# Kernel optimization log

Measured on AMD Instinct MI355X. Metric: run time of the kernel, lower is better.

## Reference

```python
import jax, jax.numpy as jnp
import numpy as np

N = 50000      # num_nodes
SEQ = 52       # seq_len (weeks)
FIN = 16       # in_channels
H = 128        # hidden_dim
E = 800000     # num edges (before self-loops)
NEG_SLOPE = 0.2


def setup_inputs() -> dict:
    key = jax.random.key(0)
    ks = jax.random.split(key, 10)
    return {
        "x_seq": jax.random.normal(ks[0], (SEQ, N, FIN), jnp.float32),
        "edge_index": jax.random.randint(ks[1], (2, E), 0, N),
        "Wg": jax.random.normal(ks[2], (FIN, H), jnp.float32) * 0.1,       # GAT linear (no bias on lin in PyG default path; bias added at end)
        "att_src": jax.random.normal(ks[3], (H,), jnp.float32) * 0.1,
        "att_dst": jax.random.normal(ks[4], (H,), jnp.float32) * 0.1,
        "bias_g": jnp.zeros((H,), jnp.float32),
        "W_ih": jax.random.normal(ks[5], (3 * H, H), jnp.float32) * 0.05,  # GRUCell input weights (r,z,n order)
        "W_hh": jax.random.normal(ks[6], (3 * H, H), jnp.float32) * 0.05,
        "b_ih": jnp.zeros((3 * H,), jnp.float32),
        "b_hh": jnp.zeros((3 * H,), jnp.float32),
        "W_fc": jax.random.normal(ks[7], (1, H), jnp.float32) * 0.1,
        "b_fc": jnp.zeros((1,), jnp.float32),
    }


def _gat(x, src, dst, Wg, att_src, att_dst, bias_g):
    # x: [N, FIN] -> xp: [N, H]
    xp = x @ Wg
    a_s = xp @ att_src  # [N]
    a_d = xp @ att_dst  # [N]
    e = jax.nn.leaky_relu(a_s[src] + a_d[dst], NEG_SLOPE)          # [E+N] edge scores
    m = jax.ops.segment_max(e, dst, num_segments=N)                # softmax over incoming edges per dst
    w = jnp.exp(e - m[dst])
    denom = jax.ops.segment_sum(w, dst, num_segments=N)
    alpha = w / denom[dst]
    out = jax.ops.segment_sum(alpha[:, None] * xp[src], dst, num_segments=N)  # [N, H]
    return out + bias_g


def _gru_cell(x, h, W_ih, W_hh, b_ih, b_hh):
    gi = x @ W_ih.T + b_ih  # [N, 3H]
    gh = h @ W_hh.T + b_hh
    i_r, i_z, i_n = jnp.split(gi, 3, axis=1)
    h_r, h_z, h_n = jnp.split(gh, 3, axis=1)
    r = jax.nn.sigmoid(i_r + h_r)
    z = jax.nn.sigmoid(i_z + h_z)
    n = jnp.tanh(i_n + r * h_n)
    return (1.0 - z) * n + z * h


def reference(x_seq, edge_index, Wg, att_src, att_dst, bias_g, W_ih, W_hh, b_ih, b_hh, W_fc, b_fc):
    # PyG GATConv add_self_loops=True
    loop = jnp.arange(N)
    src = jnp.concatenate([edge_index[0], loop])
    dst = jnp.concatenate([edge_index[1], loop])

    def step(h, xt):
        spatial = jax.nn.relu(_gat(xt, src, dst, Wg, att_src, att_dst, bias_g))
        h_new = _gru_cell(spatial, h, W_ih, W_hh, b_ih, b_hh)
        return h_new, None

    h0 = jnp.zeros((N, H), jnp.float32)
    hT, _ = jax.lax.scan(step, h0, x_seq)
    return hT @ W_fc.T + b_fc  # [N, 1]
```

## Files before the change

kernel.cpp:

```cpp
#include <hip/hip_runtime.h>
#include <math.h>

#define NN 50000
#define SEQ 52
#define FIN 16
#define HD 128
#define NEG_SLOPE 0.2f

typedef short bf16x8 __attribute__((ext_vector_type(8)));
typedef float f32x16 __attribute__((ext_vector_type(16)));

__device__ __forceinline__ short f2bf(float x) {
    unsigned u = __float_as_uint(x);
    u += 0x7fffu + ((u >> 16) & 1u);
    return (short)(u >> 16);
}
__device__ __forceinline__ float b2f(short s) {
    return __uint_as_float(((unsigned)(unsigned short)s) << 16);
}

__global__ void deg_init_kernel(int* deg, int n) {
    int i = blockIdx.x * blockDim.x + threadIdx.x;
    if (i < n) deg[i] = 1;
}

__global__ void deg_count_kernel(const int* __restrict__ dst, int* deg, int e) {
    int i = blockIdx.x * blockDim.x + threadIdx.x;
    if (i < e) atomicAdd(&deg[dst[i]], 1);
}

__global__ __launch_bounds__(1024) void scan_kernel(const int* __restrict__ deg,
                                                    int* row_ptr, int n) {
    __shared__ int buf[1024];
    __shared__ int carry;
    int tid = threadIdx.x;
    if (tid == 0) carry = 0;
    __syncthreads();
    for (int base = 0; base < n; base += 1024) {
        int i = base + tid;
        int v = (i < n) ? deg[i] : 0;
        buf[tid] = v;
        __syncthreads();
        for (int off = 1; off < 1024; off <<= 1) {
            int t = (tid >= off) ? buf[tid - off] : 0;
            __syncthreads();
            buf[tid] += t;
            __syncthreads();
        }
        if (i < n) row_ptr[i] = carry + buf[tid] - v;
        __syncthreads();
        if (tid == 1023) carry += buf[1023];
        __syncthreads();
    }
    if (tid == 0) row_ptr[n] = carry;
}

__global__ void selfloop_kernel(const int* __restrict__ row_ptr, int* cursor,
                                int* col, int n) {
    int i = blockIdx.x * blockDim.x + threadIdx.x;
    if (i < n) {
        int p = row_ptr[i];
        col[p] = i;
        cursor[i] = p + 1;
    }
}

__global__ void scatter_kernel(const int* __restrict__ src, const int* __restrict__ dst,
                               int* cursor, int* col, int e) {
    int i = blockIdx.x * blockDim.x + threadIdx.x;
    if (i < e) {
        int p = atomicAdd(&cursor[dst[i]], 1);
        col[p] = src[i];
    }
}

__global__ void wpack_kernel(const float* __restrict__ Wi, const float* __restrict__ Wh,
                             short* __restrict__ wfrag) {
    int idx = blockIdx.x * blockDim.x + threadIdx.x;
    if (idx >= 3 * 4 * 8 * 4 * 64) return;
    int lane = idx & 63;
    int which = (idx >> 6) & 3;
    int ks = (idx >> 8) & 7;
    int slab = (idx >> 11) & 3;
    int g = idx >> 13;
    int col = slab * 32 + (lane & 31);
    int kcol = ks * 16 + (lane >> 5) * 8;
    const float* Wsrc = (which < 2) ? Wi : Wh;
    const float* row = Wsrc + (size_t)(g * HD + col) * HD + kcol;
    short* dstp = wfrag + (size_t)idx * 8;
    bool lo = (which & 1);
#pragma unroll
    for (int e = 0; e < 8; ++e) {
        float v = row[e];
        short hi = f2bf(v);
        dstp[e] = lo ? f2bf(v - b2f(hi)) : hi;
    }
}


__global__ __launch_bounds__(256) void xp_kernel(
    const float* __restrict__ x, const float* __restrict__ Wg,
    const float* __restrict__ att_src, const float* __restrict__ att_dst,
    unsigned* __restrict__ xpb, float* __restrict__ a_s, float* __restrict__ a_d, int n) {
    int wave = (blockIdx.x * blockDim.x + threadIdx.x) >> 6;
    int lane = threadIdx.x & 63;
    if (wave >= n) return;
    const float* xr = x + (size_t)wave * FIN;
    float xv[FIN];
#pragma unroll
    for (int k = 0; k < FIN; ++k) xv[k] = xr[k];
    int c0 = 2 * lane, c1 = 2 * lane + 1;
    float v0 = 0.f, v1 = 0.f;
#pragma unroll
    for (int k = 0; k < FIN; ++k) {
        v0 += xv[k] * Wg[k * HD + c0];
        v1 += xv[k] * Wg[k * HD + c1];
    }
    unsigned p = (unsigned)(unsigned short)f2bf(v0) |
                 ((unsigned)(unsigned short)f2bf(v1) << 16);
    xpb[(size_t)wave * 64 + lane] = p;
    float s = v0 * att_src[c0] + v1 * att_src[c1];
    float d = v0 * att_dst[c0] + v1 * att_dst[c1];
#pragma unroll
    for (int off = 32; off; off >>= 1) {
        s += __shfl_xor(s, off);
        d += __shfl_xor(d, off);
    }
    if (lane == 0) { a_s[wave] = s; a_d[wave] = d; }
}

__global__ __launch_bounds__(256, 4) void gatgru_kernel(
    const int* __restrict__ row_ptr, const int* __restrict__ col,
    const float* __restrict__ a_s, const float* __restrict__ a_d,
    const short* __restrict__ xpb, const float* __restrict__ bias_g,
    float* __restrict__ h, const short* __restrict__ wfrag,
    const float* __restrict__ b_ih, const float* __restrict__ b_hh, int n,
    const float* __restrict__ x_next, const float* __restrict__ Wg,
    const float* __restrict__ att_src, const float* __restrict__ att_dst,
    unsigned* __restrict__ xpb_next, float* __restrict__ a_s_next,
    float* __restrict__ a_d_next) {
    __shared__ bf16x8 sSH[512];
    __shared__ bf16x8 sSL[512];
    __shared__ bf16x8 sHH[512];
    __shared__ bf16x8 sHL[512];

    int t = threadIdx.x;
    int lane = t & 63;
    int w = t >> 6;
    int n0 = blockIdx.x * 32;

    float h8[2][8];
#pragma unroll
    for (int q = 0; q < 2; ++q) {
        int ks = w * 2 + q;
        int row = n0 + (lane & 31);
        if (row >= n) row = n - 1;
        int kcol = ks * 16 + (lane >> 5) * 8;
        const float* hp = h + (size_t)row * HD + kcol;
        *(float4*)(h8[q]) = *(const float4*)(hp);
        *(float4*)(h8[q] + 4) = *(const float4*)(hp + 4);
    }

    int g = t >> 4;
    int fg = t & 15;
    int glane = lane & 0x30;

#pragma unroll
    for (int nn = 0; nn < 2; ++nn) {
        int nl = g + nn * 16;
        int nd = n0 + nl;
        int sidx = (fg >> 1) * 64 + (fg & 1) * 32 + nl;
        if (nd < n) {
            int start = row_ptr[nd], end = row_ptr[nd + 1];
            float ad = a_d[nd];
            float acc[8] = {0.f, 0.f, 0.f, 0.f, 0.f, 0.f, 0.f, 0.f};
            float dpart = 0.f;
            for (int base = start; base < end; base += 16) {
                int cnt = end - base;
                if (cnt > 16) cnt = 16;
                int s = 0;
                float wgt = 0.f;
                if (fg < cnt) {
                    s = col[base + fg];
                    float e = a_s[s] + ad;
                    e = (e > 0.f) ? e : NEG_SLOPE * e;
                    wgt = __expf(e);
                }
                dpart += wgt;
                for (int k = 0; k < cnt; k += 4) {
                    int si[4];
                    float wt[4];
#pragma unroll
                    for (int u = 0; u < 4; ++u) {
                        int c = k + u;
                        int cc = (c < cnt) ? c : 0;
                        si[u] = __shfl(s, glane | cc);
                        wt[u] = __shfl(wgt, glane | cc);
                        if (c >= cnt) wt[u] = 0.f;
                    }
                    bf16x8 r[4];
#pragma unroll
                    for (int u = 0; u < 4; ++u)
                        r[u] = *(const bf16x8*)(xpb + (size_t)si[u] * HD + fg * 8);
#pragma unroll
                    for (int u = 0; u < 4; ++u)
#pragma unroll
                        for (int j = 0; j < 8; ++j) acc[j] += wt[u] * b2f(r[u][j]);
                }
            }
            dpart += __shfl_xor(dpart, 8);
            dpart += __shfl_xor(dpart, 4);
            dpart += __shfl_xor(dpart, 2);
            dpart += __shfl_xor(dpart, 1);
            float inv = __fdividef(1.f, dpart);
            bf16x8 sh, sl;
#pragma unroll
            for (int j = 0; j < 8; ++j) {
                float o = acc[j] * inv + bias_g[fg * 8 + j];
                o = fmaxf(o, 0.f);
                short hi = f2bf(o);
                sh[j] = hi;
                sl[j] = f2bf(o - b2f(hi));
            }
            sSH[sidx] = sh;
            sSL[sidx] = sl;
        } else {
            bf16x8 z;
#pragma unroll
            for (int j = 0; j < 8; ++j) z[j] = 0;
            sSH[sidx] = z;
            sSL[sidx] = z;
        }
    }

#pragma unroll
    for (int q = 0; q < 2; ++q) {
        int ks = w * 2 + q;
        bf16x8 hh, hl;
#pragma unroll
        for (int j = 0; j < 8; ++j) {
            short b = f2bf(h8[q][j]);
            hh[j] = b;
            hl[j] = f2bf(h8[q][j] - b2f(b));
        }
        int li = ks * 64 + lane;
        sHH[li] = hh;
        sHL[li] = hl;
    }
    __syncthreads();

    int j0 = w * 32;
    int cj = lane & 31;
    int kh = lane >> 5;

    const short* wb = wfrag + (size_t)w * 16384 + (size_t)lane * 8;

    f32x16 arz0, arz1;
#pragma unroll
    for (int r = 0; r < 16; ++r) { arz0[r] = 0.f; arz1[r] = 0.f; }

#pragma unroll
    for (int ks = 0; ks < 8; ++ks) {
        int li = ks * 64 + lane;
        bf16x8 aSH = sSH[li];
        bf16x8 aSL = sSL[li];
        bf16x8 aHH = sHH[li];
        bf16x8 aHL = sHL[li];
        {
            const short* p = wb + 0 * 65536 + ks * 2048;
            bf16x8 wih = *(const bf16x8*)(p);
            bf16x8 wil = *(const bf16x8*)(p + 512);
            bf16x8 whh = *(const bf16x8*)(p + 1024);
            bf16x8 whl = *(const bf16x8*)(p + 1536);
            arz0 = __builtin_amdgcn_mfma_f32_32x32x16_bf16(aSH, wih, arz0, 0, 0, 0);
            arz0 = __builtin_amdgcn_mfma_f32_32x32x16_bf16(aHH, whh, arz0, 0, 0, 0);
            arz0 = __builtin_amdgcn_mfma_f32_32x32x16_bf16(aSL, wih, arz0, 0, 0, 0);
            arz0 = __builtin_amdgcn_mfma_f32_32x32x16_bf16(aHL, whh, arz0, 0, 0, 0);
            arz0 = __builtin_amdgcn_mfma_f32_32x32x16_bf16(aSH, wil, arz0, 0, 0, 0);
            arz0 = __builtin_amdgcn_mfma_f32_32x32x16_bf16(aHH, whl, arz0, 0, 0, 0);
        }
        {
            const short* p = wb + 1 * 65536 + ks * 2048;
            bf16x8 wih = *(const bf16x8*)(p);
            bf16x8 wil = *(const bf16x8*)(p + 512);
            bf16x8 whh = *(const bf16x8*)(p + 1024);
            bf16x8 whl = *(const bf16x8*)(p + 1536);
            arz1 = __builtin_amdgcn_mfma_f32_32x32x16_bf16(aSH, wih, arz1, 0, 0, 0);
            arz1 = __builtin_amdgcn_mfma_f32_32x32x16_bf16(aHH, whh, arz1, 0, 0, 0);
            arz1 = __builtin_amdgcn_mfma_f32_32x32x16_bf16(aSL, wih, arz1, 0, 0, 0);
            arz1 = __builtin_amdgcn_mfma_f32_32x32x16_bf16(aHL, whh, arz1, 0, 0, 0);
            arz1 = __builtin_amdgcn_mfma_f32_32x32x16_bf16(aSH, wil, arz1, 0, 0, 0);
            arz1 = __builtin_amdgcn_mfma_f32_32x32x16_bf16(aHH, whl, arz1, 0, 0, 0);
        }
    }

    f32x16 ain, ahn;
#pragma unroll
    for (int r = 0; r < 16; ++r) { ain[r] = 0.f; ahn[r] = 0.f; }

#pragma unroll
    for (int ks = 0; ks < 8; ++ks) {
        int li = ks * 64 + lane;
        bf16x8 aSH = sSH[li];
        bf16x8 aSL = sSL[li];
        bf16x8 aHH = sHH[li];
        bf16x8 aHL = sHL[li];
        const short* p = wb + 2 * 65536 + ks * 2048;
        bf16x8 wih = *(const bf16x8*)(p);
        bf16x8 wil = *(const bf16x8*)(p + 512);
        bf16x8 whh = *(const bf16x8*)(p + 1024);
        bf16x8 whl = *(const bf16x8*)(p + 1536);
        ain = __builtin_amdgcn_mfma_f32_32x32x16_bf16(aSH, wih, ain, 0, 0, 0);
        ahn = __builtin_amdgcn_mfma_f32_32x32x16_bf16(aHH, whh, ahn, 0, 0, 0);
        ain = __builtin_amdgcn_mfma_f32_32x32x16_bf16(aSL, wih, ain, 0, 0, 0);
        ahn = __builtin_amdgcn_mfma_f32_32x32x16_bf16(aHL, whh, ahn, 0, 0, 0);
        ain = __builtin_amdgcn_mfma_f32_32x32x16_bf16(aSH, wil, ain, 0, 0, 0);
        ahn = __builtin_amdgcn_mfma_f32_32x32x16_bf16(aHH, whl, ahn, 0, 0, 0);
    }

    int j = j0 + cj;
    float brz0 = b_ih[j] + b_hh[j];
    float brz1 = b_ih[HD + j] + b_hh[HD + j];
    float bin_ = b_ih[2 * HD + j];
    float bhn = b_hh[2 * HD + j];
    const short* hhs = (const short*)sHH;
    const short* hls = (const short*)sHL;
    int ksj = j >> 4, halfj = (j >> 3) & 1, ej = j & 7;

#pragma unroll
    for (int r = 0; r < 16; ++r) {
        int nl = (r & 3) + 8 * (r >> 2) + 4 * kh;
        int node = n0 + nl;
        if (node < n) {
            float rr = __fdividef(1.f, 1.f + __expf(-(arz0[r] + brz0)));
            float zz = __fdividef(1.f, 1.f + __expf(-(arz1[r] + brz1)));
            float u = ain[r] + bin_ + rr * (ahn[r] + bhn);
            float ex = __expf(2.f * u);
            float nn2 = 1.f - __fdividef(2.f, ex + 1.f);
            int li = (ksj * 64 + nl + 32 * halfj) * 8 + ej;
            float hold = b2f(hhs[li]) + b2f(hls[li]);
            h[(size_t)node * HD + j] = (1.f - zz) * nn2 + zz * hold;
        }
    }

    if (x_next != nullptr) {
        int node = n0 + (t >> 3);
        int sub = t & 7;
        if (node < n) {
            const float* xr = x_next + (size_t)node * FIN;
            float xv[FIN];
#pragma unroll
            for (int k = 0; k < FIN; ++k) xv[k] = xr[k];
            float s = 0.f, d = 0.f;
            unsigned pk[8];
#pragma unroll
            for (int c = 0; c < 16; c += 2) {
                int c0 = sub * 16 + c, c1 = c0 + 1;
                float v0 = 0.f, v1 = 0.f;
#pragma unroll
                for (int k = 0; k < FIN; ++k) {
                    v0 += xv[k] * Wg[k * HD + c0];
                    v1 += xv[k] * Wg[k * HD + c1];
                }
                s += v0 * att_src[c0] + v1 * att_src[c1];
                d += v0 * att_dst[c0] + v1 * att_dst[c1];
                pk[c >> 1] = (unsigned)(unsigned short)f2bf(v0) |
                             ((unsigned)(unsigned short)f2bf(v1) << 16);
            }
            unsigned* dstw = xpb_next + (size_t)node * 64 + sub * 8;
            *(uint4*)(dstw) = make_uint4(pk[0], pk[1], pk[2], pk[3]);
            *(uint4*)(dstw + 4) = make_uint4(pk[4], pk[5], pk[6], pk[7]);
            s += __shfl_xor(s, 1); s += __shfl_xor(s, 2); s += __shfl_xor(s, 4);
            d += __shfl_xor(d, 1); d += __shfl_xor(d, 2); d += __shfl_xor(d, 4);
            if (sub == 0) { a_s_next[node] = s; a_d_next[node] = d; }
        }
    }
}

__global__ __launch_bounds__(256) void fc_kernel(
    const float* __restrict__ h, const float* __restrict__ W_fc,
    const float* __restrict__ b_fc, float* __restrict__ out, int n) {
    int wave = (blockIdx.x * blockDim.x + threadIdx.x) >> 6;
    int lane = threadIdx.x & 63;
    if (wave >= n) return;
    float v = h[(size_t)wave * HD + lane] * W_fc[lane] +
              h[(size_t)wave * HD + lane + 64] * W_fc[lane + 64];
#pragma unroll
    for (int off = 32; off; off >>= 1) v += __shfl_xor(v, off);
    if (lane == 0) out[wave] = v + b_fc[0];
}

extern "C" void kernel_launch(void* const* d_in, const int* in_sizes, int n_in,
                              void* d_out, int out_size, void* d_ws, size_t ws_size,
                              hipStream_t stream) {
    const float* x_seq   = (const float*)d_in[0];
    const int*   ei      = (const int*)d_in[1];
    const float* Wg      = (const float*)d_in[2];
    const float* att_src = (const float*)d_in[3];
    const float* att_dst = (const float*)d_in[4];
    const float* bias_g  = (const float*)d_in[5];
    const float* W_ih    = (const float*)d_in[6];
    const float* W_hh    = (const float*)d_in[7];
    const float* b_ih    = (const float*)d_in[8];
    const float* b_hh    = (const float*)d_in[9];
    const float* W_fc    = (const float*)d_in[10];
    const float* b_fc    = (const float*)d_in[11];
    float* out = (float*)d_out;

    const int N = NN;
    const int E = in_sizes[1] / 2;
    const int* src = ei;
    const int* dst = ei + E;

    char* w = (char*)d_ws;
    size_t off = 0;
    auto alloc = [&](size_t bytes) {
        char* p = w + off;
        off = (off + bytes + 255) & ~(size_t)255;
        return p;
    };
    int*   deg     = (int*)alloc((size_t)N * 4);
    int*   row_ptr = (int*)alloc((size_t)(N + 1) * 4);
    int*   cursor  = (int*)alloc((size_t)N * 4);
    int*   col     = (int*)alloc((size_t)(E + N) * 4);
    float* a_s0    = (float*)alloc((size_t)N * 4);
    float* a_d0    = (float*)alloc((size_t)N * 4);
    float* a_s1    = (float*)alloc((size_t)N * 4);
    float* a_d1    = (float*)alloc((size_t)N * 4);
    unsigned* xpb0 = (unsigned*)alloc((size_t)N * 64 * 4);
    unsigned* xpb1 = (unsigned*)alloc((size_t)N * 64 * 4);
    float* hbuf    = (float*)alloc((size_t)N * HD * 4);
    short* wfrag   = (short*)alloc((size_t)3 * 4 * 8 * 4 * 64 * 8 * 2);

    unsigned* xpbs[2] = {xpb0, xpb1};
    float* a_ss[2] = {a_s0, a_s1};
    float* a_ds[2] = {a_d0, a_d1};

    hipMemsetAsync(hbuf, 0, (size_t)N * HD * 4, stream);

    deg_init_kernel<<<(N + 255) / 256, 256, 0, stream>>>(deg, N);
    deg_count_kernel<<<(E + 255) / 256, 256, 0, stream>>>(dst, deg, E);
    scan_kernel<<<1, 1024, 0, stream>>>(deg, row_ptr, N);
    selfloop_kernel<<<(N + 255) / 256, 256, 0, stream>>>(row_ptr, cursor, col, N);
    scatter_kernel<<<(E + 255) / 256, 256, 0, stream>>>(src, dst, cursor, col, E);
    wpack_kernel<<<(24576 + 255) / 256, 256, 0, stream>>>(W_ih, W_hh, wfrag);

    int node_wave_blocks = (N * 64 + 255) / 256;
    int fused_blocks = (N + 31) / 32;

    xp_kernel<<<node_wave_blocks, 256, 0, stream>>>(x_seq, Wg, att_src, att_dst,
                                                    xpb0, a_s0, a_d0, N);

    for (int t = 0; t < SEQ; ++t) {
        int cur = t & 1, nxt = cur ^ 1;
        const float* xnext = (t + 1 < SEQ) ? (x_seq + (size_t)(t + 1) * N * FIN)
                                           : nullptr;
        gatgru_kernel<<<fused_blocks, 256, 0, stream>>>(
            row_ptr, col, a_ss[cur], a_ds[cur], (const short*)xpbs[cur], bias_g,
            hbuf, wfrag, b_ih, b_hh, N,
            xnext, Wg, att_src, att_dst, xpbs[nxt], a_ss[nxt], a_ds[nxt]);
    }
    fc_kernel<<<node_wave_blocks, 256, 0, stream>>>(hbuf, W_fc, b_fc, out, N);
}
```

Before: 5.701 ms.

## Stage per-block edge weights in LDS once instead of per 16-lane group

At the start of each fused GAT+GRU block, all edges of the block's 32 destination nodes are loaded cooperatively into shared memory as (src, exp score) pairs, using a new dst_slot array built during CSR construction. The aggregation loop then reads indices and weights from LDS instead of recomputing them with per-lane gathers and shuffles, and computes the denominator in-thread. A fallback keeps the old path when a block has more than ECAP edges. The GRU epilogue also reloads the old h from global memory instead of reconstructing it from the bf16 hi/lo LDS copies. This costs extra LDS (6 KB), a block barrier, and an extra global read of dst_slot.

```diff
diff --git a/kernel.cpp b/kernel.cpp
--- a/kernel.cpp
+++ b/kernel.cpp
@@ -6,6 +6,7 @@
 #define FIN 16
 #define HD 128
 #define NEG_SLOPE 0.2f
+#define ECAP 768
 
 typedef short bf16x8 __attribute__((ext_vector_type(8)));
 typedef float f32x16 __attribute__((ext_vector_type(16)));
@@ -56,21 +57,24 @@
 }
 
 __global__ void selfloop_kernel(const int* __restrict__ row_ptr, int* cursor,
-                                int* col, int n) {
+                                int* col, int* dst_slot, int n) {
     int i = blockIdx.x * blockDim.x + threadIdx.x;
     if (i < n) {
         int p = row_ptr[i];
         col[p] = i;
+        dst_slot[p] = i;
         cursor[i] = p + 1;
     }
 }
 
 __global__ void scatter_kernel(const int* __restrict__ src, const int* __restrict__ dst,
-                               int* cursor, int* col, int e) {
+                               int* cursor, int* col, int* dst_slot, int e) {
     int i = blockIdx.x * blockDim.x + threadIdx.x;
     if (i < e) {
-        int p = atomicAdd(&cursor[dst[i]], 1);
+        int d = dst[i];
+        int p = atomicAdd(&cursor[d], 1);
         col[p] = src[i];
+        dst_slot[p] = d;
     }
 }
 
@@ -131,6 +135,7 @@
 
 __global__ __launch_bounds__(256, 4) void gatgru_kernel(
     const int* __restrict__ row_ptr, const int* __restrict__ col,
+    const int* __restrict__ dst_slot,
     const float* __restrict__ a_s, const float* __restrict__ a_d,
     const short* __restrict__ xpb, const float* __restrict__ bias_g,
     float* __restrict__ h, const short* __restrict__ wfrag,
@@ -143,6 +148,7 @@
     __shared__ bf16x8 sSL[512];
     __shared__ bf16x8 sHH[512];
     __shared__ bf16x8 sHL[512];
+    __shared__ uint2  sE[ECAP];
 
     int t = threadIdx.x;
     int lane = t & 63;
@@ -161,6 +167,21 @@
         *(float4*)(h8[q] + 4) = *(const float4*)(hp + 4);
     }
 
+    int nend = (n0 + 32 < n) ? (n0 + 32) : n;
+    int rp0 = row_ptr[n0];
+    int ecnt = row_ptr[nend] - rp0;
+    bool staged = (ecnt <= ECAP);
+    if (staged) {
+        for (int p = t; p < ecnt; p += 256) {
+            int gp = rp0 + p;
+            int s = col[gp];
+            float e = a_s[s] + a_d[dst_slot[gp]];
+            e = (e > 0.f) ? e : NEG_SLOPE * e;
+            sE[p] = make_uint2((unsigned)s, __float_as_uint(__expf(e)));
+        }
+    }
+    __syncthreads();
+
     int g = t >> 4;
     int fg = t & 15;
     int glane = lane & 0x30;
@@ -172,47 +193,75 @@
         int sidx = (fg >> 1) * 64 + (fg & 1) * 32 + nl;
         if (nd < n) {
             int start = row_ptr[nd], end = row_ptr[nd + 1];
-            float ad = a_d[nd];
             float acc[8] = {0.f, 0.f, 0.f, 0.f, 0.f, 0.f, 0.f, 0.f};
-            float dpart = 0.f;
-            for (int base = start; base < end; base += 16) {
-                int cnt = end - base;
-                if (cnt > 16) cnt = 16;
-                int s = 0;
-                float wgt = 0.f;
-                if (fg < cnt) {
-                    s = col[base + fg];
-                    float e = a_s[s] + ad;
-                    e = (e > 0.f) ? e : NEG_SLOPE * e;
-                    wgt = __expf(e);
-                }
-                dpart += wgt;
+            float denom = 0.f;
+            if (staged) {
+                int s0 = start - rp0;
+                int cnt = end - start;
                 for (int k = 0; k < cnt; k += 4) {
                     int si[4];
                     float wt[4];
 #pragma unroll
                     for (int u = 0; u < 4; ++u) {
                         int c = k + u;
-                        int cc = (c < cnt) ? c : 0;
-                        si[u] = __shfl(s, glane | cc);
-                        wt[u] = __shfl(wgt, glane | cc);
-                        if (c >= cnt) wt[u] = 0.f;
+                        uint2 ew = sE[s0 + ((c < cnt) ? c : 0)];
+                        si[u] = (int)ew.x;
+                        wt[u] = (c < cnt) ? __uint_as_float(ew.y) : 0.f;
                     }
                     bf16x8 r[4];
 #pragma unroll
                     for (int u = 0; u < 4; ++u)
                         r[u] = *(const bf16x8*)(xpb + (size_t)si[u] * HD + fg * 8);
 #pragma unroll
-                    for (int u = 0; u < 4; ++u)
+                    for (int u = 0; u < 4; ++u) {
+                        denom += wt[u];
 #pragma unroll
                         for (int j = 0; j < 8; ++j) acc[j] += wt[u] * b2f(r[u][j]);
+                    }
                 }
+            } else {
+                float ad = a_d[nd];
+                float dpart = 0.f;
+                for (int base = start; base < end; base += 16) {
+                    int cnt = end - base;
+                    if (cnt > 16) cnt = 16;
+                    int s = 0;
+                    float wgt = 0.f;
+                    if (fg < cnt) {
+                        s = col[base + fg];
+                        float e = a_s[s] + ad;
+                        e = (e > 0.f) ? e : NEG_SLOPE * e;
+                        wgt = __expf(e);
+                    }
+                    dpart += wgt;
+                    for (int k = 0; k < cnt; k += 4) {
+                        int si[4];
+                        float wt[4];
+#pragma unroll
+                        for (int u = 0; u < 4; ++u) {
+                            int c = k + u;
+                            int cc = (c < cnt) ? c : 0;
+                            si[u] = __shfl(s, glane | cc);
+                            wt[u] = __shfl(wgt, glane | cc);
+                            if (c >= cnt) wt[u] = 0.f;
+                        }
+                        bf16x8 r[4];
+#pragma unroll
+                        for (int u = 0; u < 4; ++u)
+                            r[u] = *(const bf16x8*)(xpb + (size_t)si[u] * HD + fg * 8);
+#pragma unroll
+                        for (int u = 0; u < 4; ++u)
+#pragma unroll
+                            for (int j = 0; j < 8; ++j) acc[j] += wt[u] * b2f(r[u][j]);
+                    }
+                }
+                dpart += __shfl_xor(dpart, 8);
+                dpart += __shfl_xor(dpart, 4);
+                dpart += __shfl_xor(dpart, 2);
+                dpart += __shfl_xor(dpart, 1);
+                denom = dpart;
             }
-            dpart += __shfl_xor(dpart, 8);
-            dpart += __shfl_xor(dpart, 4);
-            dpart += __shfl_xor(dpart, 2);
-            dpart += __shfl_xor(dpart, 1);
-            float inv = __fdividef(1.f, dpart);
+            float inv = __fdividef(1.f, denom);
             bf16x8 sh, sl;
 #pragma unroll
             for (int j = 0; j < 8; ++j) {
@@ -323,22 +372,18 @@
     float brz1 = b_ih[HD + j] + b_hh[HD + j];
     float bin_ = b_ih[2 * HD + j];
     float bhn = b_hh[2 * HD + j];
-    const short* hhs = (const short*)sHH;
-    const short* hls = (const short*)sHL;
-    int ksj = j >> 4, halfj = (j >> 3) & 1, ej = j & 7;
 
 #pragma unroll
     for (int r = 0; r < 16; ++r) {
         int nl = (r & 3) + 8 * (r >> 2) + 4 * kh;
         int node = n0 + nl;
         if (node < n) {
+            float hold = h[(size_t)node * HD + j];
             float rr = __fdividef(1.f, 1.f + __expf(-(arz0[r] + brz0)));
             float zz = __fdividef(1.f, 1.f + __expf(-(arz1[r] + brz1)));
             float u = ain[r] + bin_ + rr * (ahn[r] + bhn);
             float ex = __expf(2.f * u);
             float nn2 = 1.f - __fdividef(2.f, ex + 1.f);
-            int li = (ksj * 64 + nl + 32 * halfj) * 8 + ej;
-            float hold = b2f(hhs[li]) + b2f(hls[li]);
             h[(size_t)node * HD + j] = (1.f - zz) * nn2 + zz * hold;
         }
     }
@@ -419,18 +464,19 @@
         off = (off + bytes + 255) & ~(size_t)255;
         return p;
     };
-    int*   deg     = (int*)alloc((size_t)N * 4);
-    int*   row_ptr = (int*)alloc((size_t)(N + 1) * 4);
-    int*   cursor  = (int*)alloc((size_t)N * 4);
-    int*   col     = (int*)alloc((size_t)(E + N) * 4);
-    float* a_s0    = (float*)alloc((size_t)N * 4);
-    float* a_d0    = (float*)alloc((size_t)N * 4);
-    float* a_s1    = (float*)alloc((size_t)N * 4);
-    float* a_d1    = (float*)alloc((size_t)N * 4);
-    unsigned* xpb0 = (unsigned*)alloc((size_t)N * 64 * 4);
-    unsigned* xpb1 = (unsigned*)alloc((size_t)N * 64 * 4);
-    float* hbuf    = (float*)alloc((size_t)N * HD * 4);
-    short* wfrag   = (short*)alloc((size_t)3 * 4 * 8 * 4 * 64 * 8 * 2);
+    int*   deg      = (int*)alloc((size_t)N * 4);
+    int*   row_ptr  = (int*)alloc((size_t)(N + 1) * 4);
+    int*   cursor   = (int*)alloc((size_t)N * 4);
+    int*   col      = (int*)alloc((size_t)(E + N) * 4);
+    int*   dst_slot = (int*)alloc((size_t)(E + N) * 4);
+    float* a_s0     = (float*)alloc((size_t)N * 4);
+    float* a_d0     = (float*)alloc((size_t)N * 4);
+    float* a_s1     = (float*)alloc((size_t)N * 4);
+    float* a_d1     = (float*)alloc((size_t)N * 4);
+    unsigned* xpb0  = (unsigned*)alloc((size_t)N * 64 * 4);
+    unsigned* xpb1  = (unsigned*)alloc((size_t)N * 64 * 4);
+    float* hbuf     = (float*)alloc((size_t)N * HD * 4);
+    short* wfrag    = (short*)alloc((size_t)3 * 4 * 8 * 4 * 64 * 8 * 2);
 
     unsigned* xpbs[2] = {xpb0, xpb1};
     float* a_ss[2] = {a_s0, a_s1};
@@ -441,8 +487,10 @@
     deg_init_kernel<<<(N + 255) / 256, 256, 0, stream>>>(deg, N);
     deg_count_kernel<<<(E + 255) / 256, 256, 0, stream>>>(dst, deg, E);
     scan_kernel<<<1, 1024, 0, stream>>>(deg, row_ptr, N);
-    selfloop_kernel<<<(N + 255) / 256, 256, 0, stream>>>(row_ptr, cursor, col, N);
-    scatter_kernel<<<(E + 255) / 256, 256, 0, stream>>>(src, dst, cursor, col, E);
+    selfloop_kernel<<<(N + 255) / 256, 256, 0, stream>>>(row_ptr, cursor, col,
+                                                         dst_slot, N);
+    scatter_kernel<<<(E + 255) / 256, 256, 0, stream>>>(src, dst, cursor, col,
+                                                        dst_slot, E);
     wpack_kernel<<<(24576 + 255) / 256, 256, 0, stream>>>(W_ih, W_hh, wfrag);
 
     int node_wave_blocks = (N * 64 + 255) / 256;
@@ -456,8 +504,8 @@
         const float* xnext = (t + 1 < SEQ) ? (x_seq + (size_t)(t + 1) * N * FIN)
                                            : nullptr;
         gatgru_kernel<<<fused_blocks, 256, 0, stream>>>(
-            row_ptr, col, a_ss[cur], a_ds[cur], (const short*)xpbs[cur], bias_g,
-            hbuf, wfrag, b_ih, b_hh, N,
+            row_ptr, col, dst_slot, a_ss[cur], a_ds[cur], (const short*)xpbs[cur],
+            bias_g, hbuf, wfrag, b_ih, b_hh, N,
             xnext, Wg, att_src, att_dst, xpbs[nxt], a_ss[nxt], a_ds[nxt]);
     }
     fc_kernel<<<node_wave_blocks, 256, 0, stream>>>(hbuf, W_fc, b_fc, out, N);
```

After: 6.154 ms. 7.9% more time.

## Bucket each node's incoming edges by source range to improve gather locality

Applied to the files above, without the earlier changes.

Builds the CSR with four sub-rows per destination node, grouped by which quarter of the node ID space the source falls in. The fused GAT/GRU kernel then walks all nodes' edges for source range 0 before moving to range 1, and so on. The aim is to keep the working set of gathered bf16 feature rows within a cache-sized slice at any moment. In exchange, each destination's edges are split into smaller chunks, so the 16-lane groups run less full, there are more loop iterations, and the preprocessing arrays and scan are four times larger.

```diff
diff --git a/kernel.cpp b/kernel.cpp
--- a/kernel.cpp
+++ b/kernel.cpp
@@ -6,6 +6,8 @@
 #define FIN 16
 #define HD 128
 #define NEG_SLOPE 0.2f
+#define NRANGE 4
+#define RDIV 12500
 
 typedef short bf16x8 __attribute__((ext_vector_type(8)));
 typedef float f32x16 __attribute__((ext_vector_type(16)));
@@ -19,14 +21,18 @@
     return __uint_as_float(((unsigned)(unsigned short)s) << 16);
 }
 
-__global__ void deg_init_kernel(int* deg, int n) {
+__global__ void deg_init_kernel(int* deg4, int n4) {
     int i = blockIdx.x * blockDim.x + threadIdx.x;
-    if (i < n) deg[i] = 1;
-}
-
-__global__ void deg_count_kernel(const int* __restrict__ dst, int* deg, int e) {
+    if (i < n4) {
+        int node = i >> 2, r = i & 3;
+        deg4[i] = (r == node / RDIV) ? 1 : 0;
+    }
+}
+
+__global__ void deg_count_kernel(const int* __restrict__ src,
+                                 const int* __restrict__ dst, int* deg4, int e) {
     int i = blockIdx.x * blockDim.x + threadIdx.x;
-    if (i < e) atomicAdd(&deg[dst[i]], 1);
+    if (i < e) atomicAdd(&deg4[dst[i] * 4 + src[i] / RDIV], 1);
 }
 
 __global__ __launch_bounds__(1024) void scan_kernel(const int* __restrict__ deg,
@@ -55,22 +61,28 @@
     if (tid == 0) row_ptr[n] = carry;
 }
 
-__global__ void selfloop_kernel(const int* __restrict__ row_ptr, int* cursor,
-                                int* col, int n) {
+__global__ void selfloop_kernel(const int* __restrict__ row_ptr4, int* cursor4,
+                                int* col, int n4) {
     int i = blockIdx.x * blockDim.x + threadIdx.x;
-    if (i < n) {
-        int p = row_ptr[i];
-        col[p] = i;
-        cursor[i] = p + 1;
+    if (i < n4) {
+        int node = i >> 2, r = i & 3;
+        int base = row_ptr4[i];
+        if (r == node / RDIV) {
+            col[base] = node;
+            cursor4[i] = base + 1;
+        } else {
+            cursor4[i] = base;
+        }
     }
 }
 
 __global__ void scatter_kernel(const int* __restrict__ src, const int* __restrict__ dst,
-                               int* cursor, int* col, int e) {
+                               int* cursor4, int* col, int e) {
     int i = blockIdx.x * blockDim.x + threadIdx.x;
     if (i < e) {
-        int p = atomicAdd(&cursor[dst[i]], 1);
-        col[p] = src[i];
+        int s = src[i];
+        int p = atomicAdd(&cursor4[dst[i] * 4 + s / RDIV], 1);
+        col[p] = s;
     }
 }
 
@@ -130,7 +142,7 @@
 }
 
 __global__ __launch_bounds__(256, 4) void gatgru_kernel(
-    const int* __restrict__ row_ptr, const int* __restrict__ col,
+    const int* __restrict__ rp4, const int* __restrict__ col,
     const float* __restrict__ a_s, const float* __restrict__ a_d,
     const short* __restrict__ xpb, const float* __restrict__ bias_g,
     float* __restrict__ h, const short* __restrict__ wfrag,
@@ -165,58 +177,78 @@
     int fg = t & 15;
     int glane = lane & 0x30;
 
+    float acc[2][8];
+    float dpart[2] = {0.f, 0.f};
+    float adv[2];
+#pragma unroll
+    for (int nn = 0; nn < 2; ++nn) {
+#pragma unroll
+        for (int j = 0; j < 8; ++j) acc[nn][j] = 0.f;
+        int nd = n0 + g + nn * 16;
+        adv[nn] = (nd < n) ? a_d[nd] : 0.f;
+    }
+
+#pragma unroll
+    for (int p = 0; p < NRANGE; ++p) {
+#pragma unroll
+        for (int nn = 0; nn < 2; ++nn) {
+            int nd = n0 + g + nn * 16;
+            if (nd < n) {
+                int start = rp4[nd * 4 + p], end = rp4[nd * 4 + p + 1];
+                for (int base = start; base < end; base += 16) {
+                    int cnt = end - base;
+                    if (cnt > 16) cnt = 16;
+                    int s = 0;
+                    float wgt = 0.f;
+                    if (fg < cnt) {
+                        s = col[base + fg];
+                        float e = a_s[s] + adv[nn];
+                        e = (e > 0.f) ? e : NEG_SLOPE * e;
+                        wgt = __expf(e);
+                    }
+                    dpart[nn] += wgt;
+                    for (int k = 0; k < cnt; k += 4) {
+                        int si[4];
+                        float wt[4];
+#pragma unroll
+                        for (int u = 0; u < 4; ++u) {
+                            int c = k + u;
+                            int cc = (c < cnt) ? c : 0;
+                            si[u] = __shfl(s, glane | cc);
+                            wt[u] = __shfl(wgt, glane | cc);
+                            if (c >= cnt) wt[u] = 0.f;
+                        }
+                        bf16x8 r[4];
+#pragma unroll
+                        for (int u = 0; u < 4; ++u)
+                            r[u] = *(const bf16x8*)(xpb + (size_t)si[u] * HD + fg * 8);
+#pragma unroll
+                        for (int u = 0; u < 4; ++u)
+#pragma unroll
+                            for (int j = 0; j < 8; ++j)
+                                acc[nn][j] += wt[u] * b2f(r[u][j]);
+                    }
+                }
+            }
+        }
+    }
+
 #pragma unroll
     for (int nn = 0; nn < 2; ++nn) {
         int nl = g + nn * 16;
         int nd = n0 + nl;
         int sidx = (fg >> 1) * 64 + (fg & 1) * 32 + nl;
         if (nd < n) {
-            int start = row_ptr[nd], end = row_ptr[nd + 1];
-            float ad = a_d[nd];
-            float acc[8] = {0.f, 0.f, 0.f, 0.f, 0.f, 0.f, 0.f, 0.f};
-            float dpart = 0.f;
-            for (int base = start; base < end; base += 16) {
-                int cnt = end - base;
-                if (cnt > 16) cnt = 16;
-                int s = 0;
-                float wgt = 0.f;
-                if (fg < cnt) {
-                    s = col[base + fg];
-                    float e = a_s[s] + ad;
-                    e = (e > 0.f) ? e : NEG_SLOPE * e;
-                    wgt = __expf(e);
-                }
-                dpart += wgt;
-                for (int k = 0; k < cnt; k += 4) {
-                    int si[4];
-                    float wt[4];
-#pragma unroll
-                    for (int u = 0; u < 4; ++u) {
-                        int c = k + u;
-                        int cc = (c < cnt) ? c : 0;
-                        si[u] = __shfl(s, glane | cc);
-                        wt[u] = __shfl(wgt, glane | cc);
-                        if (c >= cnt) wt[u] = 0.f;
-                    }
-                    bf16x8 r[4];
-#pragma unroll
-                    for (int u = 0; u < 4; ++u)
-                        r[u] = *(const bf16x8*)(xpb + (size_t)si[u] * HD + fg * 8);
-#pragma unroll
-                    for (int u = 0; u < 4; ++u)
-#pragma unroll
-                        for (int j = 0; j < 8; ++j) acc[j] += wt[u] * b2f(r[u][j]);
-                }
-            }
-            dpart += __shfl_xor(dpart, 8);
-            dpart += __shfl_xor(dpart, 4);
-            dpart += __shfl_xor(dpart, 2);
-            dpart += __shfl_xor(dpart, 1);
-            float inv = __fdividef(1.f, dpart);
+            float dp = dpart[nn];
+            dp += __shfl_xor(dp, 8);
+            dp += __shfl_xor(dp, 4);
+            dp += __shfl_xor(dp, 2);
+            dp += __shfl_xor(dp, 1);
+            float inv = __fdividef(1.f, dp);
             bf16x8 sh, sl;
 #pragma unroll
             for (int j = 0; j < 8; ++j) {
-                float o = acc[j] * inv + bias_g[fg * 8 + j];
+                float o = acc[nn][j] * inv + bias_g[fg * 8 + j];
                 o = fmaxf(o, 0.f);
                 short hi = f2bf(o);
                 sh[j] = hi;
@@ -419,9 +451,9 @@
         off = (off + bytes + 255) & ~(size_t)255;
         return p;
     };
-    int*   deg     = (int*)alloc((size_t)N * 4);
-    int*   row_ptr = (int*)alloc((size_t)(N + 1) * 4);
-    int*   cursor  = (int*)alloc((size_t)N * 4);
+    int*   deg4    = (int*)alloc((size_t)N * 4 * 4);
+    int*   rp4     = (int*)alloc(((size_t)N * 4 + 1) * 4);
+    int*   cursor4 = (int*)alloc((size_t)N * 4 * 4);
     int*   col     = (int*)alloc((size_t)(E + N) * 4);
     float* a_s0    = (float*)alloc((size_t)N * 4);
     float* a_d0    = (float*)alloc((size_t)N * 4);
@@ -438,11 +470,12 @@
 
     hipMemsetAsync(hbuf, 0, (size_t)N * HD * 4, stream);
 
-    deg_init_kernel<<<(N + 255) / 256, 256, 0, stream>>>(deg, N);
-    deg_count_kernel<<<(E + 255) / 256, 256, 0, stream>>>(dst, deg, E);
-    scan_kernel<<<1, 1024, 0, stream>>>(deg, row_ptr, N);
-    selfloop_kernel<<<(N + 255) / 256, 256, 0, stream>>>(row_ptr, cursor, col, N);
-    scatter_kernel<<<(E + 255) / 256, 256, 0, stream>>>(src, dst, cursor, col, E);
+    int n4 = N * 4;
+    deg_init_kernel<<<(n4 + 255) / 256, 256, 0, stream>>>(deg4, n4);
+    deg_count_kernel<<<(E + 255) / 256, 256, 0, stream>>>(src, dst, deg4, E);
+    scan_kernel<<<1, 1024, 0, stream>>>(deg4, rp4, n4);
+    selfloop_kernel<<<(n4 + 255) / 256, 256, 0, stream>>>(rp4, cursor4, col, n4);
+    scatter_kernel<<<(E + 255) / 256, 256, 0, stream>>>(src, dst, cursor4, col, E);
     wpack_kernel<<<(24576 + 255) / 256, 256, 0, stream>>>(W_ih, W_hh, wfrag);
 
     int node_wave_blocks = (N * 64 + 255) / 256;
@@ -456,7 +489,7 @@
         const float* xnext = (t + 1 < SEQ) ? (x_seq + (size_t)(t + 1) * N * FIN)
                                            : nullptr;
         gatgru_kernel<<<fused_blocks, 256, 0, stream>>>(
-            row_ptr, col, a_ss[cur], a_ds[cur], (const short*)xpbs[cur], bias_g,
+            rp4, col, a_ss[cur], a_ds[cur], (const short*)xpbs[cur], bias_g,
             hbuf, wfrag, b_ih, b_hh, N,
             xnext, Wg, att_src, att_dst, xpbs[nxt], a_ss[nxt], a_ds[nxt]);
     }
```

After: 6.428 ms. 12.8% more time.
